# Optimization experiments

Hardware: AMD Instinct MI355X
Metric: run time of the kernel (lower is better)

Reference implementation:

```python
import jax, jax.numpy as jnp
import numpy as np

N, M, D = 8192, 8192, 256
GAMMA = 1.0 / D  # standard RBF bandwidth gamma = 1/D


def setup_inputs() -> dict:
    key = jax.random.key(0)
    kx, ks = jax.random.split(key)
    x = jax.random.normal(kx, (N, D), dtype=jnp.float32)
    support = jax.random.normal(ks, (M, D), dtype=jnp.float32)
    return {"x": x, "support": support}


def reference(x, support):
    # Vectorized RBF Gram matrix: K[i, j] = exp(-gamma * ||x_i - s_j||^2)
    # ||x_i - s_j||^2 = ||x_i||^2 + ||s_j||^2 - 2 x_i . s_j  (cdist-style, one GEMM)
    x_sq = jnp.sum(x * x, axis=-1, keepdims=True)            # [N, 1]
    s_sq = jnp.sum(support * support, axis=-1)[None, :]      # [1, M]
    cross = jnp.einsum('nd,md->nm', x, support)              # [N, M]
    sq_dists = jnp.maximum(x_sq + s_sq - 2.0 * cross, 0.0)   # clamp fp error
    return jnp.exp(-GAMMA * sq_dists)
```

## Files before the change

kernel.cpp:

```cpp
#include <hip/hip_runtime.h>

#define N 8192
#define M 8192
#define D 256

typedef unsigned short ushort_t;
typedef __attribute__((ext_vector_type(8))) short short8;
typedef __attribute__((ext_vector_type(4))) float floatx4;

__device__ __forceinline__ unsigned short f2bf(float f) {
  unsigned int u = __float_as_uint(f);
  u += 0x7fffu + ((u >> 16) & 1u);
  return (unsigned short)(u >> 16);
}

__global__ __launch_bounds__(256) void prep_kernel(const float* __restrict__ x,
                                                   const float* __restrict__ s,
                                                   ushort_t* __restrict__ xb,
                                                   ushort_t* __restrict__ sb,
                                                   float* __restrict__ xn,
                                                   float* __restrict__ sn) {
  int gw = blockIdx.x * 4 + (threadIdx.x >> 6);
  int lane = threadIdx.x & 63;
  const float* src;
  ushort_t* dst;
  float* nrm;
  int row;
  if (gw < N) { src = x; dst = xb; nrm = xn; row = gw; }
  else        { src = s; dst = sb; nrm = sn; row = gw - N; }
  float4 v = ((const float4*)(src + (size_t)row * D))[lane];
  float ss = v.x * v.x + v.y * v.y + v.z * v.z + v.w * v.w;
  ushort4 o;
  o.x = f2bf(v.x); o.y = f2bf(v.y); o.z = f2bf(v.z); o.w = f2bf(v.w);
  int lr = row & 127;
  size_t off = (size_t)(row >> 7) * 65536 + (size_t)(lane >> 4) * 16384
             + (size_t)lr * 128
             + (size_t)(((((lane >> 1) & 7) ^ (lr & 7)) * 16) + (lane & 1) * 8);
  *(ushort4*)((char*)dst + off) = o;
#pragma unroll
  for (int offs = 32; offs > 0; offs >>= 1) ss += __shfl_down(ss, offs);
  if (lane == 0) nrm[row] = ss;
}

template <int P>
__device__ __forceinline__ void phase_compute(const ushort_t* As, const ushort_t* Bs,
                                              floatx4 (&acc)[4][4], int wr, int wc,
                                              int q4, int m16) {
#pragma unroll
  for (int cc = 0; cc < 2; ++cc) {
    short8 a_frag[4], b_frag[4];
#pragma unroll
    for (int i = 0; i < 4; ++i) {
      const int row = wr + i * 16 + m16;
      a_frag[i] = *(const short8*)(As + P * 8192 + row * 64 +
                                   (((cc * 4 + q4) ^ (row & 7)) << 3));
    }
#pragma unroll
    for (int j = 0; j < 4; ++j) {
      const int row = wc + j * 16 + m16;
      b_frag[j] = *(const short8*)(Bs + P * 8192 + row * 64 +
                                   (((cc * 4 + q4) ^ (row & 7)) << 3));
    }
#pragma unroll
    for (int i = 0; i < 4; ++i)
#pragma unroll
      for (int j = 0; j < 4; ++j)
        acc[i][j] = __builtin_amdgcn_mfma_f32_16x16x32_bf16(a_frag[i], b_frag[j],
                                                            acc[i][j], 0, 0, 0);
  }
}

__global__ __launch_bounds__(256, 1) void rbf_gemm(const ushort_t* __restrict__ X,
                                                   const ushort_t* __restrict__ S,
                                                   const float* __restrict__ xn,
                                                   const float* __restrict__ sn,
                                                   float* __restrict__ out) {
  __shared__ __attribute__((aligned(16))) ushort_t As[4 * 128 * 64];
  __shared__ __attribute__((aligned(16))) ushort_t Bs[4 * 128 * 64];
  __shared__ float nS[256];

  const int tid = threadIdx.x;
  const int lane = tid & 63;
  const int wave = tid >> 6;

  const int wg = blockIdx.y * 64 + blockIdx.x;
  const int swz = (wg & 7) * 512 + (wg >> 3);
  const int by = swz >> 6;
  const int bx = swz & 63;

  {
    const float* np = (tid < 128) ? (xn + by * 128 + tid)
                                  : (sn + bx * 128 + (tid - 128));
    nS[tid] = *np;
  }

  const char* gA = (const char*)X + (size_t)by * 65536 + wave * 4096 + lane * 16;
  const char* gB = (const char*)S + (size_t)bx * 65536 + wave * 4096 + lane * 16;
  char* lA = (char*)As + wave * 4096;
  char* lB = (char*)Bs + wave * 4096;
#pragma unroll
  for (int p = 0; p < 4; ++p) {
#pragma unroll
    for (int i = 0; i < 4; ++i)
      __builtin_amdgcn_global_load_lds(
          (const __attribute__((address_space(1))) void*)(gA + p * 16384 + i * 1024),
          (__attribute__((address_space(3))) void*)(lA + p * 16384 + i * 1024), 16, 0, 0);
#pragma unroll
    for (int i = 0; i < 4; ++i)
      __builtin_amdgcn_global_load_lds(
          (const __attribute__((address_space(1))) void*)(gB + p * 16384 + i * 1024),
          (__attribute__((address_space(3))) void*)(lB + p * 16384 + i * 1024), 16, 0, 0);
  }

  const int wr = (wave >> 1) * 64;
  const int wc = (wave & 1) * 64;
  const int q4 = lane >> 4;
  const int m16 = lane & 15;

  floatx4 acc[4][4];
#pragma unroll
  for (int i = 0; i < 4; ++i)
#pragma unroll
    for (int j = 0; j < 4; ++j) acc[i][j] = (floatx4){0.f, 0.f, 0.f, 0.f};

  asm volatile("s_waitcnt vmcnt(24) lgkmcnt(0)" ::: "memory");
  __builtin_amdgcn_s_barrier();
  __builtin_amdgcn_sched_barrier(0);
  phase_compute<0>(As, Bs, acc, wr, wc, q4, m16);

  asm volatile("s_waitcnt vmcnt(16)" ::: "memory");
  __builtin_amdgcn_s_barrier();
  __builtin_amdgcn_sched_barrier(0);
  phase_compute<1>(As, Bs, acc, wr, wc, q4, m16);

  asm volatile("s_waitcnt vmcnt(8)" ::: "memory");
  __builtin_amdgcn_s_barrier();
  __builtin_amdgcn_sched_barrier(0);
  phase_compute<2>(As, Bs, acc, wr, wc, q4, m16);

  asm volatile("s_waitcnt vmcnt(0)" ::: "memory");
  __builtin_amdgcn_s_barrier();
  __builtin_amdgcn_sched_barrier(0);
  phase_compute<3>(As, Bs, acc, wr, wc, q4, m16);

  const float cexp = -1.0f / (float)D;
#pragma unroll
  for (int i = 0; i < 4; ++i) {
#pragma unroll
    for (int j = 0; j < 4; ++j) {
#pragma unroll
      for (int r = 0; r < 4; ++r) {
        const int rl = wr + i * 16 + q4 * 4 + r;
        const int cl = wc + j * 16 + m16;
        float sq = nS[rl] + nS[128 + cl] - 2.0f * acc[i][j][r];
        sq = fmaxf(sq, 0.0f);
        out[(size_t)(by * 128 + rl) * M + (bx * 128 + cl)] = __expf(cexp * sq);
      }
    }
  }
}

extern "C" void kernel_launch(void* const* d_in, const int* in_sizes, int n_in,
                              void* d_out, int out_size, void* d_ws, size_t ws_size,
                              hipStream_t stream) {
  const float* x = (const float*)d_in[0];
  const float* s = (const float*)d_in[1];
  float* out = (float*)d_out;
  char* ws = (char*)d_ws;
  ushort_t* xb = (ushort_t*)ws;
  ushort_t* sb = (ushort_t*)(ws + (size_t)N * D * 2);
  float* xn = (float*)(ws + (size_t)(N + M) * D * 2);
  float* sn = xn + N;

  prep_kernel<<<(N + M) / 4, 256, 0, stream>>>(x, s, xb, sb, xn, sn);
  dim3 grid(M / 128, N / 128);
  rbf_gemm<<<grid, 256, 0, stream>>>(xb, sb, xn, sn, out);
}
```

Measured before the change: 320.5 us.

## Double-buffer LDS K-chunks to fit two blocks per CU, use nontemporal stores

Cuts LDS from four full K-chunk buffers to a two-slot ping-pong, so the kernel needs about half the shared memory. Launch bounds are raised to allow two workgroups per CU, letting one block's epilogue and stores overlap with another's loads and MFMA work. The output writes become nontemporal stores so the large fp32 result stream does not pollute the cache. The cost is extra barriers and less prefetch depth inside each block, plus possible register pressure from the higher occupancy target.

```diff
diff --git a/kernel.cpp b/kernel.cpp
--- a/kernel.cpp
+++ b/kernel.cpp
@@ -42,8 +42,8 @@
   if (lane == 0) nrm[row] = ss;
 }
 
-template <int P>
-__device__ __forceinline__ void phase_compute(const ushort_t* As, const ushort_t* Bs,
+__device__ __forceinline__ void compute_round(const ushort_t* __restrict__ As,
+                                              const ushort_t* __restrict__ Bs,
                                               floatx4 (&acc)[4][4], int wr, int wc,
                                               int q4, int m16) {
 #pragma unroll
@@ -52,14 +52,12 @@
 #pragma unroll
     for (int i = 0; i < 4; ++i) {
       const int row = wr + i * 16 + m16;
-      a_frag[i] = *(const short8*)(As + P * 8192 + row * 64 +
-                                   (((cc * 4 + q4) ^ (row & 7)) << 3));
+      a_frag[i] = *(const short8*)(As + row * 64 + (((cc * 4 + q4) ^ (row & 7)) << 3));
     }
 #pragma unroll
     for (int j = 0; j < 4; ++j) {
       const int row = wc + j * 16 + m16;
-      b_frag[j] = *(const short8*)(Bs + P * 8192 + row * 64 +
-                                   (((cc * 4 + q4) ^ (row & 7)) << 3));
+      b_frag[j] = *(const short8*)(Bs + row * 64 + (((cc * 4 + q4) ^ (row & 7)) << 3));
     }
 #pragma unroll
     for (int i = 0; i < 4; ++i)
@@ -70,13 +68,27 @@
   }
 }
 
-__global__ __launch_bounds__(256, 1) void rbf_gemm(const ushort_t* __restrict__ X,
+__device__ __forceinline__ void stage_round(const char* gA, const char* gB,
+                                            char* lA, char* lB) {
+#pragma unroll
+  for (int i = 0; i < 4; ++i)
+    __builtin_amdgcn_global_load_lds(
+        (const __attribute__((address_space(1))) void*)(gA + i * 1024),
+        (__attribute__((address_space(3))) void*)(lA + i * 1024), 16, 0, 0);
+#pragma unroll
+  for (int i = 0; i < 4; ++i)
+    __builtin_amdgcn_global_load_lds(
+        (const __attribute__((address_space(1))) void*)(gB + i * 1024),
+        (__attribute__((address_space(3))) void*)(lB + i * 1024), 16, 0, 0);
+}
+
+__global__ __launch_bounds__(256, 2) void rbf_gemm(const ushort_t* __restrict__ X,
                                                    const ushort_t* __restrict__ S,
                                                    const float* __restrict__ xn,
                                                    const float* __restrict__ sn,
                                                    float* __restrict__ out) {
-  __shared__ __attribute__((aligned(16))) ushort_t As[4 * 128 * 64];
-  __shared__ __attribute__((aligned(16))) ushort_t Bs[4 * 128 * 64];
+  __shared__ __attribute__((aligned(16))) ushort_t As[2][128 * 64];
+  __shared__ __attribute__((aligned(16))) ushort_t Bs[2][128 * 64];
   __shared__ float nS[256];
 
   const int tid = threadIdx.x;
@@ -93,24 +105,14 @@
                                   : (sn + bx * 128 + (tid - 128));
     nS[tid] = *np;
   }
+  __builtin_amdgcn_sched_barrier(0);
 
   const char* gA = (const char*)X + (size_t)by * 65536 + wave * 4096 + lane * 16;
   const char* gB = (const char*)S + (size_t)bx * 65536 + wave * 4096 + lane * 16;
-  char* lA = (char*)As + wave * 4096;
-  char* lB = (char*)Bs + wave * 4096;
-#pragma unroll
-  for (int p = 0; p < 4; ++p) {
-#pragma unroll
-    for (int i = 0; i < 4; ++i)
-      __builtin_amdgcn_global_load_lds(
-          (const __attribute__((address_space(1))) void*)(gA + p * 16384 + i * 1024),
-          (__attribute__((address_space(3))) void*)(lA + p * 16384 + i * 1024), 16, 0, 0);
-#pragma unroll
-    for (int i = 0; i < 4; ++i)
-      __builtin_amdgcn_global_load_lds(
-          (const __attribute__((address_space(1))) void*)(gB + p * 16384 + i * 1024),
-          (__attribute__((address_space(3))) void*)(lB + p * 16384 + i * 1024), 16, 0, 0);
-  }
+  char* lA0 = (char*)&As[0][0] + wave * 4096;
+  char* lB0 = (char*)&Bs[0][0] + wave * 4096;
+  char* lA1 = (char*)&As[1][0] + wave * 4096;
+  char* lB1 = (char*)&Bs[1][0] + wave * 4096;
 
   const int wr = (wave >> 1) * 64;
   const int wc = (wave & 1) * 64;
@@ -123,25 +125,32 @@
 #pragma unroll
     for (int j = 0; j < 4; ++j) acc[i][j] = (floatx4){0.f, 0.f, 0.f, 0.f};
 
-  asm volatile("s_waitcnt vmcnt(24) lgkmcnt(0)" ::: "memory");
+  stage_round(gA, gB, lA0, lB0);
+
+  stage_round(gA + 16384, gB + 16384, lA1, lB1);
+  asm volatile("s_waitcnt vmcnt(8) lgkmcnt(0)" ::: "memory");
   __builtin_amdgcn_s_barrier();
   __builtin_amdgcn_sched_barrier(0);
-  phase_compute<0>(As, Bs, acc, wr, wc, q4, m16);
+  compute_round(As[0], Bs[0], acc, wr, wc, q4, m16);
+  __builtin_amdgcn_s_barrier();
 
-  asm volatile("s_waitcnt vmcnt(16)" ::: "memory");
-  __builtin_amdgcn_s_barrier();
-  __builtin_amdgcn_sched_barrier(0);
-  phase_compute<1>(As, Bs, acc, wr, wc, q4, m16);
-
+  stage_round(gA + 2 * 16384, gB + 2 * 16384, lA0, lB0);
   asm volatile("s_waitcnt vmcnt(8)" ::: "memory");
   __builtin_amdgcn_s_barrier();
   __builtin_amdgcn_sched_barrier(0);
-  phase_compute<2>(As, Bs, acc, wr, wc, q4, m16);
+  compute_round(As[1], Bs[1], acc, wr, wc, q4, m16);
+  __builtin_amdgcn_s_barrier();
+
+  stage_round(gA + 3 * 16384, gB + 3 * 16384, lA1, lB1);
+  asm volatile("s_waitcnt vmcnt(8)" ::: "memory");
+  __builtin_amdgcn_s_barrier();
+  __builtin_amdgcn_sched_barrier(0);
+  compute_round(As[0], Bs[0], acc, wr, wc, q4, m16);
 
   asm volatile("s_waitcnt vmcnt(0)" ::: "memory");
   __builtin_amdgcn_s_barrier();
   __builtin_amdgcn_sched_barrier(0);
-  phase_compute<3>(As, Bs, acc, wr, wc, q4, m16);
+  compute_round(As[1], Bs[1], acc, wr, wc, q4, m16);
 
   const float cexp = -1.0f / (float)D;
 #pragma unroll
@@ -154,7 +163,9 @@
         const int cl = wc + j * 16 + m16;
         float sq = nS[rl] + nS[128 + cl] - 2.0f * acc[i][j][r];
         sq = fmaxf(sq, 0.0f);
-        out[(size_t)(by * 128 + rl) * M + (bx * 128 + cl)] = __expf(cexp * sq);
+        __builtin_nontemporal_store(
+            __expf(cexp * sq),
+            out + (size_t)(by * 128 + rl) * M + (bx * 128 + cl));
       }
     }
   }
```

Measured after the change: 317.8 us. About the same (-0.8%).
